# Kernel optimization log

Measured on AMD Instinct MI355X. Metric: run time of the kernel, lower is better.

## Reference

```python
import jax, jax.numpy as jnp
import numpy as np

N, K, D, L = 4096, 64, 1024, 16384  # tokens, top-k, d_in, num_latents


def setup_inputs() -> dict:
    key = jax.random.key(0)
    ks = jax.random.split(key, 9)
    x = jax.random.normal(ks[0], (N, D), jnp.float32)
    y = jax.random.normal(ks[1], (N, D), jnp.float32)
    latent_acts = jax.random.uniform(ks[2], (N, K), jnp.float32)  # post-topk acts (nonneg)
    latent_indices = jax.random.randint(ks[3], (N, K), 0, L)
    W_dec = jax.random.normal(ks[4], (L, D), jnp.float32) / np.sqrt(D).astype(np.float32)
    b_dec = jax.random.normal(ks[5], (D,), jnp.float32) * 0.01
    post_enc = jax.random.normal(ks[6], (L,), jnp.float32) * 0.01
    post_enc_scale = 1.0 + 0.1 * jax.random.normal(ks[7], (L,), jnp.float32)
    W_skip = jax.random.normal(ks[8], (D, D), jnp.float32) / np.sqrt(D).astype(np.float32)
    return {
        "x": x, "y": y,
        "latent_acts": latent_acts, "latent_indices": latent_indices,
        "W_dec": W_dec, "b_dec": b_dec,
        "post_enc": post_enc, "post_enc_scale": post_enc_scale,
        "W_skip": W_skip,
    }


def reference(x, y, latent_acts, latent_indices, W_dec, b_dec, post_enc, post_enc_scale, W_skip):
    # current_latent_acts: per-index bias gather + indexed scaling
    acts = (latent_acts + post_enc[latent_indices]) * post_enc_scale[latent_indices]  # [N,K]
    # decode: gather W_dec rows by top-k indices, weighted combine, add decoder bias
    sae_out = jnp.einsum('nk,nkd->nd', acts, W_dec[latent_indices]) + b_dec  # [N,D]
    # skip connection: x @ W_skip.mT
    sae_out = sae_out + x @ W_skip.T
    # FVU loss
    e = y - sae_out
    total_variance = jnp.sum((y - jnp.mean(y, axis=0)) ** 2)
    fvu = jnp.sum(e ** 2) / total_variance
    return sae_out, fvu
```

## Files before the change

### kernel.cpp

```cpp
#include <hip/hip_runtime.h>
#include <hip/hip_bf16.h>
#include <cstdint>

#define N_TOK 4096
#define KTOP  64
#define DIM   1024
#define NLAT  16384
#define NCHUNK 8

typedef __bf16 bf16x8 __attribute__((ext_vector_type(8)));
typedef float  floatx4 __attribute__((ext_vector_type(4)));

#define GLOBAL_AS(p) ((const __attribute__((address_space(1))) void*)(p))
#define LDS_AS(p)    ((__attribute__((address_space(3))) void*)(p))

__device__ inline unsigned short f2bf(float f){
  unsigned int u = __float_as_uint(f);
  unsigned int r = (u + 0x7fffu + ((u >> 16) & 1u)) >> 16;
  return (unsigned short)r;
}
__device__ inline float bflo(unsigned int u){ return __uint_as_float(u << 16); }
__device__ inline float bfhi(unsigned int u){ return __uint_as_float(u & 0xffff0000u); }

__global__ __launch_bounds__(256) void prep(
    const float* __restrict__ x, const float* __restrict__ Wsk,
    const float* __restrict__ Wd, const float* __restrict__ y,
    unsigned short* __restrict__ xb, unsigned short* __restrict__ wb,
    unsigned short* __restrict__ wdc,
    float* __restrict__ colsum, float* __restrict__ sumsq){
  const int b = blockIdx.x;
  const int t = threadIdx.x;
  if (b < 1024){
    int i0 = b * 1024 + t;
    #pragma unroll
    for (int i = 0; i < 4; i++){
      float4 v = ((const float4*)x)[i0 + i * 256];
      ushort4 o; o.x = f2bf(v.x); o.y = f2bf(v.y); o.z = f2bf(v.z); o.w = f2bf(v.w);
      ((ushort4*)xb)[i0 + i * 256] = o;
    }
  } else if (b < 1280){
    int i0 = (b - 1024) * 1024 + t;
    #pragma unroll
    for (int i = 0; i < 4; i++){
      float4 v = ((const float4*)Wsk)[i0 + i * 256];
      ushort4 o; o.x = f2bf(v.x); o.y = f2bf(v.y); o.z = f2bf(v.z); o.w = f2bf(v.w);
      ((ushort4*)wb)[i0 + i * 256] = o;
    }
  } else if (b < 3328){
    int lat0 = (b - 1280) * 8;
    const int chunk = t >> 5;
    const int off   = (t & 31) * 4;
    for (int r = 0; r < 8; r++){
      int lat = lat0 + r;
      float4 v = ((const float4*)(Wd + (size_t)lat * DIM))[t];
      ushort4 o; o.x = f2bf(v.x); o.y = f2bf(v.y); o.z = f2bf(v.z); o.w = f2bf(v.w);
      *(ushort4*)(wdc + ((size_t)chunk * NLAT + lat) * 128 + off) = o;
    }
  } else {
    const int r0 = (b - 3328) * 32;
    float4 cs = {0.f, 0.f, 0.f, 0.f};
    float sq = 0.f;
    for (int r = 0; r < 32; r++){
      float4 v = ((const float4*)(y + (size_t)(r0 + r) * DIM))[t];
      cs.x += v.x; cs.y += v.y; cs.z += v.z; cs.w += v.w;
      sq += v.x*v.x + v.y*v.y + v.z*v.z + v.w*v.w;
    }
    atomicAdd(&colsum[t*4+0], cs.x);
    atomicAdd(&colsum[t*4+1], cs.y);
    atomicAdd(&colsum[t*4+2], cs.z);
    atomicAdd(&colsum[t*4+3], cs.w);
    #pragma unroll
    for (int off = 32; off > 0; off >>= 1) sq += __shfl_down(sq, off, 64);
    __shared__ float s_red[4];
    if ((t & 63) == 0) s_red[t >> 6] = sq;
    __syncthreads();
    if (t == 0) atomicAdd(sumsq, s_red[0] + s_red[1] + s_red[2] + s_red[3]);
  }
}

__global__ __launch_bounds__(256) void skip_gemm(
    const unsigned short* __restrict__ xb,
    const unsigned short* __restrict__ wb,
    const float* __restrict__ b_dec,
    float* __restrict__ out){
  __shared__ unsigned short As[128][32];
  __shared__ unsigned short Bs[64][32];
  const int row0 = blockIdx.x * 128;
  const int col0 = blockIdx.y * 64;
  const int t    = threadIdx.x;
  const int lane = t & 63;
  const int w    = t >> 6;
  const int wr   = w * 32;
  const int lm   = lane & 15;
  const int kq   = lane >> 4;
  const int sr   = t >> 2;
  const int sc   = (t & 3) * 8;

  floatx4 acc[2][4] = {};

  for (int k0 = 0; k0 < DIM; k0 += 32){
    __builtin_amdgcn_global_load_lds(GLOBAL_AS(xb + (size_t)(row0 + sr) * DIM + k0 + sc),
                                     LDS_AS(&As[sr][sc]), 16, 0, 0);
    __builtin_amdgcn_global_load_lds(GLOBAL_AS(xb + (size_t)(row0 + 64 + sr) * DIM + k0 + sc),
                                     LDS_AS(&As[64 + sr][sc]), 16, 0, 0);
    __builtin_amdgcn_global_load_lds(GLOBAL_AS(wb + (size_t)(col0 + sr) * DIM + k0 + sc),
                                     LDS_AS(&Bs[sr][sc]), 16, 0, 0);
    __syncthreads();
    bf16x8 af[2], bfr[4];
    #pragma unroll
    for (int mi = 0; mi < 2; mi++) af[mi] = *(const bf16x8*)(&As[wr + mi * 16 + lm][kq * 8]);
    #pragma unroll
    for (int ni = 0; ni < 4; ni++) bfr[ni] = *(const bf16x8*)(&Bs[ni * 16 + lm][kq * 8]);
    #pragma unroll
    for (int mi = 0; mi < 2; mi++)
      #pragma unroll
      for (int ni = 0; ni < 4; ni++)
        acc[mi][ni] = __builtin_amdgcn_mfma_f32_16x16x32_bf16(af[mi], bfr[ni], acc[mi][ni], 0, 0, 0);
    __syncthreads();
  }

  const int rq = (lane >> 4) * 4;
  #pragma unroll
  for (int mi = 0; mi < 2; mi++){
    #pragma unroll
    for (int ni = 0; ni < 4; ni++){
      int col = col0 + ni * 16 + lm;
      float bd = b_dec[col];
      #pragma unroll
      for (int r = 0; r < 4; r++){
        int row = row0 + wr + mi * 16 + rq + r;
        out[(size_t)row * DIM + col] = acc[mi][ni][r] + bd;
      }
    }
  }
}

__global__ __launch_bounds__(256) void decode_residual(
    const float* __restrict__ y,
    const float* __restrict__ la,
    const int*   __restrict__ li,
    const unsigned short* __restrict__ Wdc,
    const float* __restrict__ pe,
    const float* __restrict__ pes,
    float* __restrict__ out,
    float* __restrict__ sse){
  const int chunk = blockIdx.x & 7;
  const int tok0  = (blockIdx.x >> 3) * 16;
  const int t  = threadIdx.x;
  const int tl = t >> 4;
  const int cl = t & 15;
  __shared__ uint2 s_ai[16][66];
  __shared__ float s_red[4];
  #pragma unroll
  for (int i = 0; i < 4; i++){
    int e = t + i * 256;
    int tok = e >> 6, k = e & 63;
    int id = li[(tok0 + tok) * KTOP + k];
    float a = (la[(tok0 + tok) * KTOP + k] + pe[id]) * pes[id];
    s_ai[tok][k] = make_uint2(__float_as_uint(a), (unsigned)id * 256u);
  }
  __syncthreads();
  const int n = tok0 + tl;
  const char* Wbase = (const char*)Wdc + (size_t)chunk * NLAT * 256 + cl * 16;
  float* op = out + (size_t)n * DIM + chunk * 128 + cl * 8;
  const float* yp = y + (size_t)n * DIM + chunk * 128 + cl * 8;
  float4 o0 = ((const float4*)op)[0], o1 = ((const float4*)op)[1];
  float4 y0 = ((const float4*)yp)[0], y1 = ((const float4*)yp)[1];
  float acc[8] = {};
  #pragma unroll 16
  for (int k = 0; k < KTOP; k++){
    uint2 p = s_ai[tl][k];
    const float a = __uint_as_float(p.x);
    const uint4 wv = *(const uint4*)(Wbase + p.y);
    acc[0] += a * bflo(wv.x); acc[1] += a * bfhi(wv.x);
    acc[2] += a * bflo(wv.y); acc[3] += a * bfhi(wv.y);
    acc[4] += a * bflo(wv.z); acc[5] += a * bfhi(wv.z);
    acc[6] += a * bflo(wv.w); acc[7] += a * bfhi(wv.w);
  }
  acc[0] += o0.x; acc[1] += o0.y; acc[2] += o0.z; acc[3] += o0.w;
  acc[4] += o1.x; acc[5] += o1.y; acc[6] += o1.z; acc[7] += o1.w;
  ((float4*)op)[0] = make_float4(acc[0], acc[1], acc[2], acc[3]);
  ((float4*)op)[1] = make_float4(acc[4], acc[5], acc[6], acc[7]);
  float e0 = y0.x - acc[0], e1 = y0.y - acc[1], e2 = y0.z - acc[2], e3 = y0.w - acc[3];
  float e4 = y1.x - acc[4], e5 = y1.y - acc[5], e6 = y1.z - acc[6], e7 = y1.w - acc[7];
  float s = e0*e0 + e1*e1 + e2*e2 + e3*e3 + e4*e4 + e5*e5 + e6*e6 + e7*e7;
  #pragma unroll
  for (int off = 32; off > 0; off >>= 1) s += __shfl_down(s, off, 64);
  if ((t & 63) == 0) s_red[t >> 6] = s;
  __syncthreads();
  if (t == 0) atomicAdd(sse, s_red[0] + s_red[1] + s_red[2] + s_red[3]);
}

__global__ __launch_bounds__(256) void fvu_kernel(
    const float* __restrict__ ws, float* __restrict__ fvu_out){
  const int t = threadIdx.x;
  float4 c = ((const float4*)(ws + 4))[t];
  float s = c.x*c.x + c.y*c.y + c.z*c.z + c.w*c.w;
  #pragma unroll
  for (int off = 32; off > 0; off >>= 1) s += __shfl_down(s, off, 64);
  __shared__ float s_red[4];
  if ((t & 63) == 0) s_red[t >> 6] = s;
  __syncthreads();
  if (t == 0){
    float ss = s_red[0] + s_red[1] + s_red[2] + s_red[3];
    float tv = ws[1] - ss / (float)N_TOK;
    fvu_out[0] = ws[0] / tv;
  }
}

extern "C" void kernel_launch(void* const* d_in, const int* in_sizes, int n_in,
                              void* d_out, int out_size, void* d_ws, size_t ws_size,
                              hipStream_t stream){
  const float* x   = (const float*)d_in[0];
  const float* y   = (const float*)d_in[1];
  const float* la  = (const float*)d_in[2];
  const int*   li  = (const int*)d_in[3];
  const float* Wd  = (const float*)d_in[4];
  const float* bd  = (const float*)d_in[5];
  const float* pe  = (const float*)d_in[6];
  const float* pes = (const float*)d_in[7];
  const float* Wsk = (const float*)d_in[8];
  float* out = (float*)d_out;

  float* accs = (float*)d_ws;
  unsigned short* xb  = (unsigned short*)((char*)d_ws + 8192);
  unsigned short* wb  = xb + (size_t)N_TOK * DIM;
  unsigned short* wdc = wb + (size_t)DIM * DIM;

  hipMemsetAsync(d_ws, 0, 8192, stream);
  prep<<<3456, 256, 0, stream>>>(x, Wsk, Wd, y, xb, wb, wdc, accs + 4, accs + 1);
  skip_gemm<<<dim3(N_TOK / 128, DIM / 64), 256, 0, stream>>>(xb, wb, bd, out);
  decode_residual<<<(N_TOK / 16) * NCHUNK, 256, 0, stream>>>(y, la, li, wdc, pe, pes, out, accs);
  fvu_kernel<<<1, 256, 0, stream>>>(accs, out + (size_t)N_TOK * DIM);
}
```

Measured before the change: 229.0 us.

## Fuse y statistics and FVU finalization into decode, precompute acts in prep

The separate pass over y for column sums and sum of squares is removed. Those statistics are now accumulated inside decode_residual from the y values it already loads, and the final FVU is computed by the last block through an atomic completion counter, which drops the fvu kernel and the memset launch. The per-token activation and index gather moves into prep and is written to a buffer. The conversions are widened to 8 elements per thread, and decode uses nontemporal loads and stores. In exchange it adds more atomics per block (128 column-sum atomics) and a last-block synchronization, and accs zeroing now depends on prep ordering.

```diff
diff --git a/kernel.cpp b/kernel.cpp
--- a/kernel.cpp
+++ b/kernel.cpp
@@ -10,6 +10,9 @@
 
 typedef __bf16 bf16x8 __attribute__((ext_vector_type(8)));
 typedef float  floatx4 __attribute__((ext_vector_type(4)));
+typedef float  f32x4   __attribute__((ext_vector_type(4)));
+typedef unsigned int   u32x2   __attribute__((ext_vector_type(2)));
+typedef unsigned short ushortx8 __attribute__((ext_vector_type(8)));
 
 #define GLOBAL_AS(p) ((const __attribute__((address_space(1))) void*)(p))
 #define LDS_AS(p)    ((__attribute__((address_space(3))) void*)(p))
@@ -22,59 +25,57 @@
 __device__ inline float bflo(unsigned int u){ return __uint_as_float(u << 16); }
 __device__ inline float bfhi(unsigned int u){ return __uint_as_float(u & 0xffff0000u); }
 
+__device__ inline void cvt8(const float* __restrict__ src, unsigned short* __restrict__ dst){
+  float4 a = ((const float4*)src)[0];
+  float4 b = ((const float4*)src)[1];
+  ushortx8 o;
+  o[0] = f2bf(a.x); o[1] = f2bf(a.y); o[2] = f2bf(a.z); o[3] = f2bf(a.w);
+  o[4] = f2bf(b.x); o[5] = f2bf(b.y); o[6] = f2bf(b.z); o[7] = f2bf(b.w);
+  *(ushortx8*)dst = o;
+}
+
 __global__ __launch_bounds__(256) void prep(
     const float* __restrict__ x, const float* __restrict__ Wsk,
-    const float* __restrict__ Wd, const float* __restrict__ y,
+    const float* __restrict__ Wd,
+    const float* __restrict__ la, const int* __restrict__ li,
+    const float* __restrict__ pe, const float* __restrict__ pes,
     unsigned short* __restrict__ xb, unsigned short* __restrict__ wb,
     unsigned short* __restrict__ wdc,
-    float* __restrict__ colsum, float* __restrict__ sumsq){
+    uint2* __restrict__ actbuf, float* __restrict__ accs){
   const int b = blockIdx.x;
   const int t = threadIdx.x;
   if (b < 1024){
-    int i0 = b * 1024 + t;
-    #pragma unroll
-    for (int i = 0; i < 4; i++){
-      float4 v = ((const float4*)x)[i0 + i * 256];
-      ushort4 o; o.x = f2bf(v.x); o.y = f2bf(v.y); o.z = f2bf(v.z); o.w = f2bf(v.w);
-      ((ushort4*)xb)[i0 + i * 256] = o;
+    #pragma unroll
+    for (int i = 0; i < 2; i++){
+      int idx = b * 4096 + i * 2048 + t * 8;
+      cvt8(x + idx, xb + idx);
     }
   } else if (b < 1280){
-    int i0 = (b - 1024) * 1024 + t;
-    #pragma unroll
-    for (int i = 0; i < 4; i++){
-      float4 v = ((const float4*)Wsk)[i0 + i * 256];
-      ushort4 o; o.x = f2bf(v.x); o.y = f2bf(v.y); o.z = f2bf(v.z); o.w = f2bf(v.w);
-      ((ushort4*)wb)[i0 + i * 256] = o;
-    }
-  } else if (b < 3328){
-    int lat0 = (b - 1280) * 8;
-    const int chunk = t >> 5;
-    const int off   = (t & 31) * 4;
-    for (int r = 0; r < 8; r++){
-      int lat = lat0 + r;
-      float4 v = ((const float4*)(Wd + (size_t)lat * DIM))[t];
-      ushort4 o; o.x = f2bf(v.x); o.y = f2bf(v.y); o.z = f2bf(v.z); o.w = f2bf(v.w);
-      *(ushort4*)(wdc + ((size_t)chunk * NLAT + lat) * 128 + off) = o;
+    #pragma unroll
+    for (int i = 0; i < 2; i++){
+      int idx = (b - 1024) * 4096 + i * 2048 + t * 8;
+      cvt8(Wsk + idx, wb + idx);
+    }
+  } else if (b < 5376){
+    const int j = t & 127;
+    const int chunk = j >> 4;
+    #pragma unroll
+    for (int i = 0; i < 2; i++){
+      int lat = (b - 1280) * 4 + i * 2 + (t >> 7);
+      cvt8(Wd + (size_t)lat * DIM + j * 8,
+           wdc + ((size_t)chunk * NLAT + lat) * 128 + (j & 15) * 8);
+    }
+  } else if (b < 5440){
+    int e0 = (b - 5376) * 4096 + t;
+    #pragma unroll
+    for (int i = 0; i < 16; i++){
+      int e = e0 + i * 256;
+      int id = li[e];
+      float a = (la[e] + pe[id]) * pes[id];
+      actbuf[e] = make_uint2(__float_as_uint(a), (unsigned)id * 256u);
     }
   } else {
-    const int r0 = (b - 3328) * 32;
-    float4 cs = {0.f, 0.f, 0.f, 0.f};
-    float sq = 0.f;
-    for (int r = 0; r < 32; r++){
-      float4 v = ((const float4*)(y + (size_t)(r0 + r) * DIM))[t];
-      cs.x += v.x; cs.y += v.y; cs.z += v.z; cs.w += v.w;
-      sq += v.x*v.x + v.y*v.y + v.z*v.z + v.w*v.w;
-    }
-    atomicAdd(&colsum[t*4+0], cs.x);
-    atomicAdd(&colsum[t*4+1], cs.y);
-    atomicAdd(&colsum[t*4+2], cs.z);
-    atomicAdd(&colsum[t*4+3], cs.w);
-    #pragma unroll
-    for (int off = 32; off > 0; off >>= 1) sq += __shfl_down(sq, off, 64);
-    __shared__ float s_red[4];
-    if ((t & 63) == 0) s_red[t >> 6] = sq;
-    __syncthreads();
-    if (t == 0) atomicAdd(sumsq, s_red[0] + s_red[1] + s_red[2] + s_red[3]);
+    for (int i = t; i < 1056; i += 256) accs[i] = 0.f;
   }
 }
 
@@ -137,35 +138,38 @@
 
 __global__ __launch_bounds__(256) void decode_residual(
     const float* __restrict__ y,
-    const float* __restrict__ la,
-    const int*   __restrict__ li,
+    const uint2* __restrict__ actbuf,
     const unsigned short* __restrict__ Wdc,
-    const float* __restrict__ pe,
-    const float* __restrict__ pes,
     float* __restrict__ out,
-    float* __restrict__ sse){
+    float* __restrict__ accs,
+    float* __restrict__ fvu_out){
   const int chunk = blockIdx.x & 7;
   const int tok0  = (blockIdx.x >> 3) * 16;
   const int t  = threadIdx.x;
   const int tl = t >> 4;
   const int cl = t & 15;
+  const int lane = t & 63, w = t >> 6;
   __shared__ uint2 s_ai[16][66];
-  __shared__ float s_red[4];
+  __shared__ float s_cs[4][16][8];
+  __shared__ float s_red[4][2];
+  __shared__ unsigned int s_last;
+
   #pragma unroll
   for (int i = 0; i < 4; i++){
     int e = t + i * 256;
-    int tok = e >> 6, k = e & 63;
-    int id = li[(tok0 + tok) * KTOP + k];
-    float a = (la[(tok0 + tok) * KTOP + k] + pe[id]) * pes[id];
-    s_ai[tok][k] = make_uint2(__float_as_uint(a), (unsigned)id * 256u);
-  }
-  __syncthreads();
+    u32x2 v = __builtin_nontemporal_load((const u32x2*)&actbuf[tok0 * KTOP + e]);
+    s_ai[e >> 6][e & 63] = make_uint2(v[0], v[1]);
+  }
   const int n = tok0 + tl;
   const char* Wbase = (const char*)Wdc + (size_t)chunk * NLAT * 256 + cl * 16;
   float* op = out + (size_t)n * DIM + chunk * 128 + cl * 8;
   const float* yp = y + (size_t)n * DIM + chunk * 128 + cl * 8;
-  float4 o0 = ((const float4*)op)[0], o1 = ((const float4*)op)[1];
-  float4 y0 = ((const float4*)yp)[0], y1 = ((const float4*)yp)[1];
+  f32x4 o0 = __builtin_nontemporal_load((const f32x4*)op);
+  f32x4 o1 = __builtin_nontemporal_load((const f32x4*)op + 1);
+  f32x4 y0 = __builtin_nontemporal_load((const f32x4*)yp);
+  f32x4 y1 = __builtin_nontemporal_load((const f32x4*)yp + 1);
+  __syncthreads();
+
   float acc[8] = {};
   #pragma unroll 16
   for (int k = 0; k < KTOP; k++){
@@ -177,34 +181,67 @@
     acc[4] += a * bflo(wv.z); acc[5] += a * bfhi(wv.z);
     acc[6] += a * bflo(wv.w); acc[7] += a * bfhi(wv.w);
   }
-  acc[0] += o0.x; acc[1] += o0.y; acc[2] += o0.z; acc[3] += o0.w;
-  acc[4] += o1.x; acc[5] += o1.y; acc[6] += o1.z; acc[7] += o1.w;
-  ((float4*)op)[0] = make_float4(acc[0], acc[1], acc[2], acc[3]);
-  ((float4*)op)[1] = make_float4(acc[4], acc[5], acc[6], acc[7]);
-  float e0 = y0.x - acc[0], e1 = y0.y - acc[1], e2 = y0.z - acc[2], e3 = y0.w - acc[3];
-  float e4 = y1.x - acc[4], e5 = y1.y - acc[5], e6 = y1.z - acc[6], e7 = y1.w - acc[7];
-  float s = e0*e0 + e1*e1 + e2*e2 + e3*e3 + e4*e4 + e5*e5 + e6*e6 + e7*e7;
-  #pragma unroll
-  for (int off = 32; off > 0; off >>= 1) s += __shfl_down(s, off, 64);
-  if ((t & 63) == 0) s_red[t >> 6] = s;
-  __syncthreads();
-  if (t == 0) atomicAdd(sse, s_red[0] + s_red[1] + s_red[2] + s_red[3]);
-}
-
-__global__ __launch_bounds__(256) void fvu_kernel(
-    const float* __restrict__ ws, float* __restrict__ fvu_out){
-  const int t = threadIdx.x;
-  float4 c = ((const float4*)(ws + 4))[t];
-  float s = c.x*c.x + c.y*c.y + c.z*c.z + c.w*c.w;
-  #pragma unroll
-  for (int off = 32; off > 0; off >>= 1) s += __shfl_down(s, off, 64);
-  __shared__ float s_red[4];
-  if ((t & 63) == 0) s_red[t >> 6] = s;
+  acc[0] += o0[0]; acc[1] += o0[1]; acc[2] += o0[2]; acc[3] += o0[3];
+  acc[4] += o1[0]; acc[5] += o1[1]; acc[6] += o1[2]; acc[7] += o1[3];
+  f32x4 r0 = {acc[0], acc[1], acc[2], acc[3]};
+  f32x4 r1 = {acc[4], acc[5], acc[6], acc[7]};
+  __builtin_nontemporal_store(r0, (f32x4*)op);
+  __builtin_nontemporal_store(r1, (f32x4*)op + 1);
+
+  float e0 = y0[0]-acc[0], e1 = y0[1]-acc[1], e2 = y0[2]-acc[2], e3 = y0[3]-acc[3];
+  float e4 = y1[0]-acc[4], e5 = y1[1]-acc[5], e6 = y1[2]-acc[6], e7 = y1[3]-acc[7];
+  float s  = e0*e0+e1*e1+e2*e2+e3*e3+e4*e4+e5*e5+e6*e6+e7*e7;
+  float sq = y0[0]*y0[0]+y0[1]*y0[1]+y0[2]*y0[2]+y0[3]*y0[3]
+           + y1[0]*y1[0]+y1[1]*y1[1]+y1[2]*y1[2]+y1[3]*y1[3];
+  float cs[8] = {y0[0], y0[1], y0[2], y0[3], y1[0], y1[1], y1[2], y1[3]};
+  #pragma unroll
+  for (int j = 0; j < 8; j++){
+    cs[j] += __shfl_xor(cs[j], 16, 64);
+    cs[j] += __shfl_xor(cs[j], 32, 64);
+  }
+  if (lane < 16){
+    #pragma unroll
+    for (int j = 0; j < 8; j++) s_cs[w][lane][j] = cs[j];
+  }
+  #pragma unroll
+  for (int off = 32; off > 0; off >>= 1){
+    s  += __shfl_down(s, off, 64);
+    sq += __shfl_down(sq, off, 64);
+  }
+  if (lane == 0){ s_red[w][0] = s; s_red[w][1] = sq; }
+  __syncthreads();
+  if (t < 128){
+    int c2 = t >> 3, j2 = t & 7;
+    atomicAdd(&accs[4 + chunk * 128 + c2 * 8 + j2],
+              s_cs[0][c2][j2] + s_cs[1][c2][j2] + s_cs[2][c2][j2] + s_cs[3][c2][j2]);
+  }
+  if (t == 0) atomicAdd(&accs[0], s_red[0][0] + s_red[1][0] + s_red[2][0] + s_red[3][0]);
+  if (t == 1) atomicAdd(&accs[1], s_red[0][1] + s_red[1][1] + s_red[2][1] + s_red[3][1]);
   __syncthreads();
   if (t == 0){
-    float ss = s_red[0] + s_red[1] + s_red[2] + s_red[3];
-    float tv = ws[1] - ss / (float)N_TOK;
-    fvu_out[0] = ws[0] / tv;
+    __threadfence();
+    unsigned int done = atomicAdd((unsigned int*)&accs[2], 1u);
+    s_last = (done == (unsigned int)(NCHUNK * (N_TOK / 16)) - 1u) ? 1u : 0u;
+  }
+  __syncthreads();
+  if (s_last){
+    __threadfence();
+    float sp = 0.f;
+    #pragma unroll
+    for (int i = 0; i < 4; i++){
+      float c = __hip_atomic_load(&accs[4 + t * 4 + i], __ATOMIC_RELAXED, __HIP_MEMORY_SCOPE_AGENT);
+      sp += c * c;
+    }
+    #pragma unroll
+    for (int off = 32; off > 0; off >>= 1) sp += __shfl_down(sp, off, 64);
+    if (lane == 0) s_red[w][0] = sp;
+    __syncthreads();
+    if (t == 0){
+      float ss    = s_red[0][0] + s_red[1][0] + s_red[2][0] + s_red[3][0];
+      float sse_v = __hip_atomic_load(&accs[0], __ATOMIC_RELAXED, __HIP_MEMORY_SCOPE_AGENT);
+      float sq_v  = __hip_atomic_load(&accs[1], __ATOMIC_RELAXED, __HIP_MEMORY_SCOPE_AGENT);
+      fvu_out[0] = sse_v / (sq_v - ss / (float)N_TOK);
+    }
   }
 }
 
@@ -226,10 +263,10 @@
   unsigned short* xb  = (unsigned short*)((char*)d_ws + 8192);
   unsigned short* wb  = xb + (size_t)N_TOK * DIM;
   unsigned short* wdc = wb + (size_t)DIM * DIM;
-
-  hipMemsetAsync(d_ws, 0, 8192, stream);
-  prep<<<3456, 256, 0, stream>>>(x, Wsk, Wd, y, xb, wb, wdc, accs + 4, accs + 1);
+  uint2* actbuf = (uint2*)(wdc + (size_t)NCHUNK * NLAT * 128);
+
+  prep<<<5441, 256, 0, stream>>>(x, Wsk, Wd, la, li, pe, pes, xb, wb, wdc, actbuf, accs);
   skip_gemm<<<dim3(N_TOK / 128, DIM / 64), 256, 0, stream>>>(xb, wb, bd, out);
-  decode_residual<<<(N_TOK / 16) * NCHUNK, 256, 0, stream>>>(y, la, li, wdc, pe, pes, out, accs);
-  fvu_kernel<<<1, 256, 0, stream>>>(accs, out + (size_t)N_TOK * DIM);
-}
+  decode_residual<<<(N_TOK / 16) * NCHUNK, 256, 0, stream>>>(y, actbuf, wdc, out, accs,
+                                                             out + (size_t)N_TOK * DIM);
+}
```

New measurement: 315.6 us. 1.38x slower.
